# Kernel tuning notes

Measured on AMD Instinct MI355X. Metric: run time of the kernel, lower is better.

Reference implementation:

```python
import jax, jax.numpy as jnp
import numpy as np

L, N, D, E, KD = 4, 40000, 128, 320000, 16
DECAY, N_ITER, EPS = 0.5, 3, 1e-5


def setup_inputs() -> dict:
    key = jax.random.key(0)
    ks = jax.random.split(key, 16)
    s = 0.05
    return {
        "x": jax.random.normal(ks[0], (L, N, D), jnp.float32),
        "edge_rows": jax.random.randint(ks[1], (E,), 0, N, jnp.int32),
        "edge_cols": jax.random.randint(ks[2], (E,), 0, N, jnp.int32),
        "edge_vals": jax.random.uniform(ks[3], (E,), jnp.float32) * 0.1,
        "sage_W": jax.random.normal(ks[4], (D, D), jnp.float32) * s,
        "sage_b": jnp.zeros((D,), jnp.float32),
        "sage_agg_W": jax.random.normal(ks[5], (D, D), jnp.float32) * s,
        "key_W": jax.random.normal(ks[6], (D, KD), jnp.float32) * s,
        "query_W": jax.random.normal(ks[7], (D, KD), jnp.float32) * s,
        "value_W": jax.random.normal(ks[8], (D, D), jnp.float32) * s,
        "attn_ln_g": jnp.ones((D,), jnp.float32),
        "attn_ln_b": jnp.zeros((D,), jnp.float32),
        "lin_W": jax.random.normal(ks[9], (D, D), jnp.float32) * s,
        "lin_b": jnp.zeros((D,), jnp.float32),
        "ln_g": jnp.ones((D,), jnp.float32),
        "ln_b": jnp.zeros((D,), jnp.float32),
    }


def _layernorm(x, g, b):
    mu = jnp.mean(x, axis=-1, keepdims=True)
    var = jnp.mean((x - mu) ** 2, axis=-1, keepdims=True)
    return (x - mu) * jax.lax.rsqrt(var + EPS) * g + b


def _spmm(rows, cols, vals, x2d):
    # sparse [N,N] @ dense [N,F]: out[r] = sum_e vals[e] * x2d[cols[e]] for rows[e]==r
    return jax.ops.segment_sum(vals[:, None] * x2d[cols], rows, num_segments=N)


def reference(x, edge_rows, edge_cols, edge_vals, sage_W, sage_b, sage_agg_W,
              key_W, query_W, value_W, attn_ln_g, attn_ln_b,
              lin_W, lin_b, ln_g, ln_b):
    # x: [L, N, D]
    x2d = jnp.transpose(x, (1, 0, 2)).reshape(N, L * D)  # [N, L*D]

    # ---- SAGEConv ----
    proj = x @ sage_W + sage_b
    agg = _spmm(edge_rows, edge_cols, edge_vals, x2d)
    agg = jnp.transpose(agg.reshape(N, L, D), (1, 0, 2)) @ sage_agg_W
    sage_out = jax.nn.silu(proj + agg)

    # ---- RetentiveAttention ----
    weights = jnp.mean((x @ key_W) * (x @ query_W), axis=-1, keepdims=True)
    x_acc = x
    cur = x2d
    for _ in range(1, N_ITER):
        cur = _spmm(edge_rows, edge_cols, edge_vals, cur * DECAY)
        xr = jnp.transpose(cur.reshape(N, L, D), (1, 0, 2))  # [L, N, D]
        weights = weights + jnp.mean((xr @ key_W) * (xr @ query_W), axis=-1, keepdims=True)
        x_acc = x_acc + xr
    attn_out = _layernorm((x_acc @ value_W) * weights, attn_ln_g, attn_ln_b)

    # ---- GPSConv fusion ----
    y = jax.nn.silu((sage_out + attn_out) @ lin_W + lin_b)
    return _layernorm(y, ln_g, ln_b)
```

## Files before the change

### kernel.cpp

```cpp
#include <hip/hip_runtime.h>
#include <math.h>

#define LL 4
#define NN 40000
#define DD 128
#define EE 320000
#define ROWS (LL*NN)
#define ND (NN*DD)
#define EPS_LN 1e-5f

typedef __attribute__((ext_vector_type(8))) short bf16x8;
typedef __attribute__((ext_vector_type(4))) short s16x4;
typedef __attribute__((ext_vector_type(4))) float f32x4;

#define OFF_CNT      0
#define OFF_ROWPTR   40000
#define OFF_ROWOFS   80004
#define OFF_CCOLS    120004
#define OFF_CVALS    440004
#define OFF_WBF      760004
#define OFF_A        829636
#define OFF_B        (OFF_A + ROWS*DD/2)
#define OFF_XBF      (OFF_B + ROWS*DD/2)

#define WB_W0  0
#define WB_W1  32768
#define WB_WV  65536
#define WB_WL  98304
#define WB_K   131072
#define WB_Q   135168
#define WB_LO_BIG 16384
#define WB_LO_KQ  2048
#define WB_LOGICAL 69632

__device__ __forceinline__ unsigned fu(float f) { union { float f; unsigned u; } v; v.f = f; return v.u; }
__device__ __forceinline__ float uf(unsigned u) { union { unsigned u; float f; } v; v.u = u; return v.f; }

__device__ __forceinline__ short f2bf(float f) {
    unsigned u = fu(f);
    unsigned r = u + 0x7fffu + ((u >> 16) & 1u);
    return (short)(r >> 16);
}
__device__ __forceinline__ float bf2f(short h) { return uf(((unsigned)(unsigned short)h) << 16); }
__device__ __forceinline__ void splitbf(float v, short& h, short& l) {
    h = f2bf(v);
    l = f2bf(v - bf2f(h));
}

__device__ __forceinline__ unsigned pack_hi(float a, float b) {
    return (fu(a) >> 16) | (fu(b) & 0xffff0000u);
}
__device__ __forceinline__ float resid(float a) {
    return a - uf(fu(a) & 0xffff0000u);
}

union FragU { bf16x8 v; unsigned u[4]; };

__global__ void k_hist(const int* __restrict__ rows, int* __restrict__ cnt) {
    int e = blockIdx.x * 256 + threadIdx.x;
    if (e < EE) atomicAdd(&cnt[rows[e]], 1);
}

__global__ __launch_bounds__(1024) void k_scan1(const int* __restrict__ cnt,
                                                int* __restrict__ row_ptr,
                                                int* __restrict__ bsum) {
    __shared__ int wtot[16];
    int tid = threadIdx.x, lane = tid & 63, wid = tid >> 6;
    int i = blockIdx.x * 1024 + tid;
    int v = (i < NN) ? cnt[i] : 0;
    int incl = v;
    #pragma unroll
    for (int off = 1; off < 64; off <<= 1) {
        int t = __shfl_up(incl, off);
        if (lane >= off) incl += t;
    }
    if (lane == 63) wtot[wid] = incl;
    __syncthreads();
    if (wid == 0) {
        int wv = (lane < 16) ? wtot[lane] : 0;
        #pragma unroll
        for (int off = 1; off < 16; off <<= 1) {
            int t = __shfl_up(wv, off);
            if (lane >= off) wv += t;
        }
        if (lane < 16) wtot[lane] = wv;
    }
    __syncthreads();
    int excl = ((wid > 0) ? wtot[wid - 1] : 0) + incl - v;
    if (i < NN) row_ptr[i] = excl;
    if (tid == 0) bsum[blockIdx.x] = wtot[15];
}

__global__ void k_scan2(const int* __restrict__ bsum, int* __restrict__ bofs) {
    int lane = threadIdx.x;
    int v = (lane < 40) ? bsum[lane] : 0;
    int incl = v;
    #pragma unroll
    for (int off = 1; off < 64; off <<= 1) {
        int t = __shfl_up(incl, off);
        if (lane >= off) incl += t;
    }
    if (lane < 40) bofs[lane] = incl - v;
    if (lane == 39) bofs[40] = incl;
}

__global__ __launch_bounds__(1024) void k_scan3(const int* __restrict__ bofs,
                                                int* __restrict__ row_ptr,
                                                int* __restrict__ row_ofs) {
    int i = blockIdx.x * 1024 + threadIdx.x;
    int add = bofs[blockIdx.x];
    if (i < NN) {
        int v = row_ptr[i] + add;
        row_ptr[i] = v;
        row_ofs[i] = v;
    }
    if (i == NN) row_ptr[NN] = bofs[40];
}

__global__ void k_scatter(const int* __restrict__ rows, const int* __restrict__ cols,
                          const float* __restrict__ vals, int* __restrict__ row_ofs,
                          int* __restrict__ csr_cols, float* __restrict__ csr_vals) {
    int e = blockIdx.x * 256 + threadIdx.x;
    if (e < EE) {
        int r = rows[e];
        int p = atomicAdd(&row_ofs[r], 1);
        csr_cols[p] = cols[e];
        csr_vals[p] = vals[e];
    }
}

__global__ __launch_bounds__(256) void k_xcast(const float* __restrict__ x, short* __restrict__ o) {
    int t = blockIdx.x * 256 + threadIdx.x;
    int n = t >> 4;
    int d8 = (t & 15) * 8;
    #pragma unroll
    for (int l = 0; l < LL; ++l) {
        const float* xp = x + (size_t)l * ND + (size_t)n * 128 + d8;
        f32x4 a = *(const f32x4*)xp;
        f32x4 b = *(const f32x4*)(xp + 4);
        bf16x8 r;
        #pragma unroll
        for (int j = 0; j < 4; ++j) { r[j] = f2bf(a[j]); r[j + 4] = f2bf(b[j]); }
        *(bf16x8*)(o + (size_t)n * 512 + l * 128 + d8) = r;
    }
}

__global__ __launch_bounds__(256) void k_spmm(const short* __restrict__ in,
                                              const int* __restrict__ row_ptr,
                                              const int* __restrict__ ccols,
                                              const float* __restrict__ cvals,
                                              short* __restrict__ out) {
    int wid = blockIdx.x * 4 + (threadIdx.x >> 6);
    int rA = wid * 2;
    int lane = threadIdx.x & 63;
    const short* inl = in + lane * 8;
    float accA[8] = {0.f,0.f,0.f,0.f,0.f,0.f,0.f,0.f};
    float accB[8] = {0.f,0.f,0.f,0.f,0.f,0.f,0.f,0.f};
    int a0 = row_ptr[rA], a1 = row_ptr[rA + 1], b1 = row_ptr[rA + 2];
    int b0 = a1;
    while (a0 + 4 <= a1 && b0 + 4 <= b1) {
        int ca[4], cb[4]; float va[4], vb[4]; bf16x8 xa[4], xb[4];
        #pragma unroll
        for (int j = 0; j < 4; ++j) {
            ca[j] = ccols[a0 + j]; va[j] = cvals[a0 + j];
            cb[j] = ccols[b0 + j]; vb[j] = cvals[b0 + j];
        }
        #pragma unroll
        for (int j = 0; j < 4; ++j) {
            xa[j] = *(const bf16x8*)(inl + (size_t)ca[j] * 512);
            xb[j] = *(const bf16x8*)(inl + (size_t)cb[j] * 512);
        }
        #pragma unroll
        for (int j = 0; j < 4; ++j)
            #pragma unroll
            for (int k = 0; k < 8; ++k) {
                accA[k] += va[j] * bf2f(xa[j][k]);
                accB[k] += vb[j] * bf2f(xb[j][k]);
            }
        a0 += 4; b0 += 4;
    }
    #pragma unroll 1
    for (int pass = 0; pass < 2; ++pass) {
        int e = pass ? b0 : a0, e1 = pass ? b1 : a1;
        float* acc = pass ? accB : accA;
        for (; e + 4 <= e1; e += 4) {
            int cc[4]; float vv[4]; bf16x8 xv[4];
            #pragma unroll
            for (int j = 0; j < 4; ++j) { cc[j] = ccols[e + j]; vv[j] = cvals[e + j]; }
            #pragma unroll
            for (int j = 0; j < 4; ++j) xv[j] = *(const bf16x8*)(inl + (size_t)cc[j] * 512);
            #pragma unroll
            for (int j = 0; j < 4; ++j)
                #pragma unroll
                for (int k = 0; k < 8; ++k) acc[k] += vv[j] * bf2f(xv[j][k]);
        }
        for (; e < e1; ++e) {
            int c = ccols[e];
            float v = cvals[e];
            bf16x8 xv = *(const bf16x8*)(inl + (size_t)c * 512);
            #pragma unroll
            for (int k = 0; k < 8; ++k) acc[k] += v * bf2f(xv[k]);
        }
    }
    bf16x8 oA, oB;
    #pragma unroll
    for (int k = 0; k < 8; ++k) { oA[k] = f2bf(accA[k]); oB[k] = f2bf(accB[k]); }
    *(bf16x8*)(out + (size_t)rA * 512 + lane * 8) = oA;
    *(bf16x8*)(out + (size_t)(rA + 1) * 512 + lane * 8) = oB;
}

__global__ void k_prep(const float* __restrict__ W0, const float* __restrict__ W1,
                       const float* __restrict__ Wv, const float* __restrict__ Wl,
                       const float* __restrict__ Kw, const float* __restrict__ Qw,
                       short* __restrict__ o) {
    int t = blockIdx.x * 256 + threadIdx.x;
    if (t >= WB_LOGICAL) return;
    float v;
    int hi_idx, lo_idx;
    if (t < 65536) {
        int m = t >> 14, idx = t & 16383;
        int nn = idx >> 7, kk = idx & 127;
        const float* M = (m == 0) ? W0 : (m == 1) ? W1 : (m == 2) ? Wv : Wl;
        v = M[kk * 128 + nn];
        hi_idx = m * 32768 + idx;
        lo_idx = hi_idx + WB_LO_BIG;
    } else {
        int t2 = t - 65536;
        int sel = t2 >> 11;
        int idx = t2 & 2047;
        int nn = idx >> 7, kk = idx & 127;
        const float* M = sel ? Qw : Kw;
        v = M[kk * 16 + nn];
        hi_idx = WB_K + sel * 4096 + idx;
        lo_idx = hi_idx + WB_LO_KQ;
    }
    short h, l;
    splitbf(v, h, l);
    o[hi_idx] = h;
    o[lo_idx] = l;
}

#define MFMA(a, b, c) __builtin_amdgcn_mfma_f32_16x16x32_bf16(a, b, c, 0, 0, 0)

__global__ __launch_bounds__(256) void k_dense(
    const float* __restrict__ x, const short* __restrict__ A, const short* __restrict__ B,
    const short* __restrict__ wbf,
    const float* __restrict__ sage_b, const float* __restrict__ attn_g,
    const float* __restrict__ attn_b, const float* __restrict__ lin_b,
    const float* __restrict__ ln_g, const float* __restrict__ ln_b,
    float* __restrict__ out)
{
    __shared__ short pv[4][2][2048];
    const int tid = threadIdx.x;
    const int w = tid >> 6;
    const int lane = tid & 63;
    const int n = lane & 15;
    const int q = lane >> 4;
    const int rowA = blockIdx.x * 64 + w * 16 + n;
    const int l = rowA / NN;
    const int node = rowA - l * NN;
    char* pB = (char*)&pv[w][0][0];
    char* vB = (char*)&pv[w][1][0];

    bf16x8 xh[4], ah[4], ch[4];
    f32x4 kx = {0,0,0,0}, qx = {0,0,0,0};
    f32x4 ka = {0,0,0,0}, qa = {0,0,0,0};
    f32x4 kb = {0,0,0,0}, qb = {0,0,0,0};

    {
        const float* xp = x + (size_t)rowA * 128 + q * 8;
        const short* ap = A + (size_t)node * 512 + l * 128 + q * 8;
        const short* bp = B + (size_t)node * 512 + l * 128 + q * 8;
        const short* Kp = wbf + WB_K + n * 128 + q * 8;
        const short* Qp = wbf + WB_Q + n * 128 + q * 8;
        #pragma unroll
        for (int s = 0; s < 4; ++s) {
            f32x4 x0 = *(const f32x4*)(xp + s * 32);
            f32x4 x1 = *(const f32x4*)(xp + s * 32 + 4);
            bf16x8 av = *(const bf16x8*)(ap + s * 32);
            bf16x8 bv = *(const bf16x8*)(bp + s * 32);

            f32x4 c0, c1;
            #pragma unroll
            for (int j = 0; j < 4; ++j) {
                c0[j] = x0[j] + 0.5f * bf2f(av[j])     + 0.25f * bf2f(bv[j]);
                c1[j] = x1[j] + 0.5f * bf2f(av[j + 4]) + 0.25f * bf2f(bv[j + 4]);
            }

            FragU fxh, fxl, fch;
            #pragma unroll
            for (int i = 0; i < 2; ++i) {
                fxh.u[i]     = pack_hi(x0[2*i], x0[2*i+1]);
                fxh.u[i + 2] = pack_hi(x1[2*i], x1[2*i+1]);
                fxl.u[i]     = pack_hi(resid(x0[2*i]), resid(x0[2*i+1]));
                fxl.u[i + 2] = pack_hi(resid(x1[2*i]), resid(x1[2*i+1]));
                fch.u[i]     = pack_hi(c0[2*i], c0[2*i+1]);
                fch.u[i + 2] = pack_hi(c1[2*i], c1[2*i+1]);
            }
            xh[s] = fxh.v; ah[s] = av; ch[s] = fch.v;

            bf16x8 bkh = *(const bf16x8*)(Kp + s * 32);
            bf16x8 bkl = *(const bf16x8*)(Kp + WB_LO_KQ + s * 32);
            bf16x8 bqh = *(const bf16x8*)(Qp + s * 32);
            bf16x8 bql = *(const bf16x8*)(Qp + WB_LO_KQ + s * 32);
            kx = MFMA(fxh.v, bkh, kx); kx = MFMA(fxl.v, bkh, kx); kx = MFMA(fxh.v, bkl, kx);
            qx = MFMA(fxh.v, bqh, qx); qx = MFMA(fxl.v, bqh, qx); qx = MFMA(fxh.v, bql, qx);
            ka = MFMA(av, bkh, ka); qa = MFMA(av, bqh, qa);
            kb = MFMA(bv, bkh, kb); qb = MFMA(bv, bqh, qb);
        }
    }

    f32x4 wts;
    #pragma unroll
    for (int r = 0; r < 4; ++r) {
        float p = kx[r] * qx[r] + 0.25f * (ka[r] * qa[r]) + 0.0625f * (kb[r] * qb[r]);
        p += __shfl_xor(p, 1);
        p += __shfl_xor(p, 2);
        p += __shfl_xor(p, 4);
        p += __shfl_xor(p, 8);
        wts[r] = p * (1.f / 16.f);
    }

    #pragma unroll 1
    for (int h = 0; h < 2; ++h) {
        f32x4 S[4];
        #pragma unroll
        for (int t = 0; t < 4; ++t) {
            float bv = sage_b[(h * 4 + t) * 16 + n];
            S[t] = (f32x4){bv, bv, bv, bv};
        }
        #pragma unroll
        for (int s = 0; s < 4; ++s) {
            #pragma unroll
            for (int t = 0; t < 4; ++t) {
                int col = (h * 4 + t) * 16 + n;
                bf16x8 w0h = *(const bf16x8*)(wbf + WB_W0 + col * 128 + s * 32 + q * 8);
                S[t] = MFMA(xh[s], w0h, S[t]);
                bf16x8 w1h = *(const bf16x8*)(wbf + WB_W1 + col * 128 + s * 32 + q * 8);
                S[t] = MFMA(ah[s], w1h, S[t]);
            }
        }
        #pragma unroll
        for (int t = 0; t < 4; ++t)
            #pragma unroll
            for (int r = 0; r < 4; ++r) {
                float v = S[t][r];
                v = v / (1.f + __expf(-v));
                int row = q * 4 + r;
                int byte = (row * 256 + ((h * 4 + t) * 16 + n) * 2) ^ ((row & 7) << 4);
                *(short*)(pB + byte) = f2bf(v);
            }
    }
    asm volatile("" ::: "memory");

    float mu_n, rs_n;
    {
        f32x4 s1 = {0,0,0,0}, s2 = {0,0,0,0};
        #pragma unroll 1
        for (int h = 0; h < 2; ++h) {
            f32x4 V[4];
            #pragma unroll
            for (int t = 0; t < 4; ++t) V[t] = (f32x4){0.f, 0.f, 0.f, 0.f};
            #pragma unroll
            for (int s = 0; s < 4; ++s)
                #pragma unroll
                for (int t = 0; t < 4; ++t) {
                    int col = (h * 4 + t) * 16 + n;
                    bf16x8 wvh = *(const bf16x8*)(wbf + WB_WV + col * 128 + s * 32 + q * 8);
                    V[t] = MFMA(ch[s], wvh, V[t]);
                }
            #pragma unroll
            for (int t = 0; t < 4; ++t)
                #pragma unroll
                for (int r = 0; r < 4; ++r) {
                    float v = V[t][r] * wts[r];
                    s1[r] += v; s2[r] += v * v;
                    int row = q * 4 + r;
                    int byte = (row * 256 + ((h * 4 + t) * 16 + n) * 2) ^ ((row & 7) << 4);
                    *(short*)(vB + byte) = f2bf(v);
                }
        }
        #pragma unroll
        for (int r = 0; r < 4; ++r) {
            float a1 = s1[r], a2 = s2[r];
            a1 += __shfl_xor(a1, 1); a2 += __shfl_xor(a2, 1);
            a1 += __shfl_xor(a1, 2); a2 += __shfl_xor(a2, 2);
            a1 += __shfl_xor(a1, 4); a2 += __shfl_xor(a2, 4);
            a1 += __shfl_xor(a1, 8); a2 += __shfl_xor(a2, 8);
            s1[r] = a1; s2[r] = a2;
        }
        float mu4[4], rs4[4];
        #pragma unroll
        for (int r = 0; r < 4; ++r) {
            mu4[r] = s1[r] * (1.f / 128.f);
            float var = s2[r] * (1.f / 128.f) - mu4[r] * mu4[r];
            rs4[r] = rsqrtf(var + EPS_LN);
        }
        int src = (n >> 2) << 4;
        float mA = __shfl(mu4[0], src), mB_ = __shfl(mu4[1], src);
        float mC = __shfl(mu4[2], src), mD = __shfl(mu4[3], src);
        float rA = __shfl(rs4[0], src), rB_ = __shfl(rs4[1], src);
        float rC = __shfl(rs4[2], src), rD = __shfl(rs4[3], src);
        float m01 = (n & 1) ? mB_ : mA, m23 = (n & 1) ? mD : mC;
        float r01 = (n & 1) ? rB_ : rA, r23 = (n & 1) ? rD : rC;
        mu_n = (n & 2) ? m23 : m01;
        rs_n = (n & 2) ? r23 : r01;
    }
    asm volatile("" ::: "memory");

    bf16x8 zh[4];
    #pragma unroll
    for (int s = 0; s < 4; ++s) {
        int byte = (n * 256 + s * 64 + q * 16) ^ ((n & 7) << 4);
        bf16x8 ph = *(const bf16x8*)(pB + byte);
        bf16x8 vh = *(const bf16x8*)(vB + byte);
        const float* gp = attn_g + s * 32 + q * 8;
        const float* bp = attn_b + s * 32 + q * 8;
        f32x4 g0 = *(const f32x4*)gp, g1 = *(const f32x4*)(gp + 4);
        f32x4 b0 = *(const f32x4*)bp, b1 = *(const f32x4*)(bp + 4);
        float z[8];
        #pragma unroll
        for (int j = 0; j < 4; ++j) {
            z[j]     = bf2f(ph[j])     + (bf2f(vh[j])     - mu_n) * rs_n * g0[j] + b0[j];
            z[j + 4] = bf2f(ph[j + 4]) + (bf2f(vh[j + 4]) - mu_n) * rs_n * g1[j] + b1[j];
        }
        FragU f;
        f.u[0] = pack_hi(z[0], z[1]); f.u[1] = pack_hi(z[2], z[3]);
        f.u[2] = pack_hi(z[4], z[5]); f.u[3] = pack_hi(z[6], z[7]);
        zh[s] = f.v;
    }
    asm volatile("" ::: "memory");

    float* fz = (float*)pB;
    f32x4 t1 = {0,0,0,0}, t2 = {0,0,0,0};
    #pragma unroll 1
    for (int h = 0; h < 2; ++h) {
        f32x4 F[4];
        #pragma unroll
        for (int t = 0; t < 4; ++t) {
            float bv = lin_b[(h * 4 + t) * 16 + n];
            F[t] = (f32x4){bv, bv, bv, bv};
        }
        #pragma unroll
        for (int s = 0; s < 4; ++s)
            #pragma unroll
            for (int t = 0; t < 4; ++t) {
                int col = (h * 4 + t) * 16 + n;
                bf16x8 wlh = *(const bf16x8*)(wbf + WB_WL + col * 128 + s * 32 + q * 8);
                F[t] = MFMA(zh[s], wlh, F[t]);
            }
        #pragma unroll
        for (int t = 0; t < 4; ++t)
            #pragma unroll
            for (int r = 0; r < 4; ++r) {
                float v = F[t][r];
                v = v / (1.f + __expf(-v));
                t1[r] += v; t2[r] += v * v;
                fz[(q * 4 + r) * 128 + (h * 4 + t) * 16 + n] = v;
            }
    }
    asm volatile("" ::: "memory");
    #pragma unroll
    for (int r = 0; r < 4; ++r) {
        float a1 = t1[r], a2 = t2[r];
        a1 += __shfl_xor(a1, 1); a2 += __shfl_xor(a2, 1);
        a1 += __shfl_xor(a1, 2); a2 += __shfl_xor(a2, 2);
        a1 += __shfl_xor(a1, 4); a2 += __shfl_xor(a2, 4);
        a1 += __shfl_xor(a1, 8); a2 += __shfl_xor(a2, 8);
        t1[r] = a1; t2[r] = a2;
    }
    #pragma unroll
    for (int t = 0; t < 8; ++t) {
        float g = ln_g[t * 16 + n];
        float bb = ln_b[t * 16 + n];
        #pragma unroll
        for (int r = 0; r < 4; ++r) {
            float mu = t1[r] * (1.f / 128.f);
            float var = t2[r] * (1.f / 128.f) - mu * mu;
            float rs = rsqrtf(var + EPS_LN);
            float v = fz[(q * 4 + r) * 128 + t * 16 + n];
            size_t row = (size_t)blockIdx.x * 64 + w * 16 + q * 4 + r;
            out[row * 128 + t * 16 + n] = (v - mu) * rs * g + bb;
        }
    }
}

extern "C" void kernel_launch(void* const* d_in, const int* in_sizes, int n_in,
                              void* d_out, int out_size, void* d_ws, size_t ws_size,
                              hipStream_t stream) {
    const float* x       = (const float*)d_in[0];
    const int*   erows   = (const int*)d_in[1];
    const int*   ecols   = (const int*)d_in[2];
    const float* evals   = (const float*)d_in[3];
    const float* sage_W  = (const float*)d_in[4];
    const float* sage_b  = (const float*)d_in[5];
    const float* sage_aW = (const float*)d_in[6];
    const float* key_W   = (const float*)d_in[7];
    const float* query_W = (const float*)d_in[8];
    const float* value_W = (const float*)d_in[9];
    const float* attn_g  = (const float*)d_in[10];
    const float* attn_b  = (const float*)d_in[11];
    const float* lin_W   = (const float*)d_in[12];
    const float* lin_b   = (const float*)d_in[13];
    const float* ln_g    = (const float*)d_in[14];
    const float* ln_b    = (const float*)d_in[15];
    float* out = (float*)d_out;

    int*   wsi = (int*)d_ws;
    float* wsf = (float*)d_ws;
    int*   cnt      = wsi + OFF_CNT;
    int*   row_ptr  = wsi + OFF_ROWPTR;
    int*   row_ofs  = wsi + OFF_ROWOFS;
    int*   csr_cols = wsi + OFF_CCOLS;
    float* csr_vals = wsf + OFF_CVALS;
    short* wbf      = (short*)(wsf + OFF_WBF);
    short* Abf      = (short*)(wsf + OFF_A);
    short* Bbf      = (short*)(wsf + OFF_B);
    short* Xbf      = (short*)(wsf + OFF_XBF);
    int*   bsum     = (int*)(wsf + OFF_A);
    int*   bofs     = bsum + 64;

    hipMemsetAsync(cnt, 0, NN * sizeof(int), stream);
    k_hist<<<(EE + 255) / 256, 256, 0, stream>>>(erows, cnt);
    k_prep<<<(WB_LOGICAL + 255) / 256, 256, 0, stream>>>(sage_W, sage_aW, value_W, lin_W,
                                                         key_W, query_W, wbf);
    k_xcast<<<NN * 16 / 256, 256, 0, stream>>>(x, Xbf);
    k_scan1<<<40, 1024, 0, stream>>>(cnt, row_ptr, bsum);
    k_scan2<<<1, 64, 0, stream>>>(bsum, bofs);
    k_scan3<<<40, 1024, 0, stream>>>(bofs, row_ptr, row_ofs);
    k_scatter<<<(EE + 255) / 256, 256, 0, stream>>>(erows, ecols, evals, row_ofs, csr_cols, csr_vals);

    k_spmm<<<NN / 8, 256, 0, stream>>>(Xbf, row_ptr, csr_cols, csr_vals, Abf);
    k_spmm<<<NN / 8, 256, 0, stream>>>(Abf, row_ptr, csr_cols, csr_vals, Bbf);

    k_dense<<<ROWS / 64, 256, 0, stream>>>(x, Abf, Bbf, wbf, sage_b, attn_g, attn_b,
                                           lin_b, ln_g, ln_b, out);
}
```

Baseline: 550.0 us.

## Pre-swizzle weights into MFMA fragment order and keep dense intermediates in registers

Weight preparation now writes bf16 weights in per-lane fragment order, so each lane loads a contiguous 16-byte chunk at lane*8 with coalesced wave-wide loads instead of strided column reads. The dense kernel computes all 8 output tiles at once rather than two halves. The SAGE and value outputs and the final activation stay in registers, and the attention layernorm is applied before a single LDS transpose of z. This removes two LDS round trips and the global re-reads of the layernorm parameters, at the cost of more live registers and possibly lower occupancy.

```diff
diff --git a/kernel.cpp b/kernel.cpp
--- a/kernel.cpp
+++ b/kernel.cpp
@@ -219,10 +219,13 @@
     int hi_idx, lo_idx;
     if (t < 65536) {
         int m = t >> 14, idx = t & 16383;
-        int nn = idx >> 7, kk = idx & 127;
+        int col = idx >> 7, kk = idx & 127;
         const float* M = (m == 0) ? W0 : (m == 1) ? W1 : (m == 2) ? Wv : Wl;
-        v = M[kk * 128 + nn];
-        hi_idx = m * 32768 + idx;
+        v = M[kk * 128 + col];
+        int tt = col >> 4, nn = col & 15;
+        int s = kk >> 5, q = (kk >> 3) & 3, j = kk & 7;
+        int fm = (tt * 4 + s) * 512 + (q * 16 + nn) * 8 + j;
+        hi_idx = m * 32768 + fm;
         lo_idx = hi_idx + WB_LO_BIG;
     } else {
         int t2 = t - 65536;
@@ -231,7 +234,9 @@
         int nn = idx >> 7, kk = idx & 127;
         const float* M = sel ? Qw : Kw;
         v = M[kk * 16 + nn];
-        hi_idx = WB_K + sel * 4096 + idx;
+        int s = kk >> 5, q = (kk >> 3) & 3, j = kk & 7;
+        int fm = s * 512 + (q * 16 + nn) * 8 + j;
+        hi_idx = WB_K + sel * 4096 + fm;
         lo_idx = hi_idx + WB_LO_KQ;
     }
     short h, l;
@@ -250,7 +255,7 @@
     const float* __restrict__ ln_g, const float* __restrict__ ln_b,
     float* __restrict__ out)
 {
-    __shared__ short pv[4][2][2048];
+    __shared__ short zs[4][16 * 128];
     const int tid = threadIdx.x;
     const int w = tid >> 6;
     const int lane = tid & 63;
@@ -259,8 +264,8 @@
     const int rowA = blockIdx.x * 64 + w * 16 + n;
     const int l = rowA / NN;
     const int node = rowA - l * NN;
-    char* pB = (char*)&pv[w][0][0];
-    char* vB = (char*)&pv[w][1][0];
+    char* zb = (char*)&zs[0][0] + w * 4096;
+    const short* wl8 = wbf + lane * 8;
 
     bf16x8 xh[4], ah[4], ch[4];
     f32x4 kx = {0,0,0,0}, qx = {0,0,0,0};
@@ -271,8 +276,6 @@
         const float* xp = x + (size_t)rowA * 128 + q * 8;
         const short* ap = A + (size_t)node * 512 + l * 128 + q * 8;
         const short* bp = B + (size_t)node * 512 + l * 128 + q * 8;
-        const short* Kp = wbf + WB_K + n * 128 + q * 8;
-        const short* Qp = wbf + WB_Q + n * 128 + q * 8;
         #pragma unroll
         for (int s = 0; s < 4; ++s) {
             f32x4 x0 = *(const f32x4*)(xp + s * 32);
@@ -299,10 +302,10 @@
             }
             xh[s] = fxh.v; ah[s] = av; ch[s] = fch.v;
 
-            bf16x8 bkh = *(const bf16x8*)(Kp + s * 32);
-            bf16x8 bkl = *(const bf16x8*)(Kp + WB_LO_KQ + s * 32);
-            bf16x8 bqh = *(const bf16x8*)(Qp + s * 32);
-            bf16x8 bql = *(const bf16x8*)(Qp + WB_LO_KQ + s * 32);
+            bf16x8 bkh = *(const bf16x8*)(wl8 + WB_K + s * 512);
+            bf16x8 bkl = *(const bf16x8*)(wl8 + WB_K + WB_LO_KQ + s * 512);
+            bf16x8 bqh = *(const bf16x8*)(wl8 + WB_Q + s * 512);
+            bf16x8 bql = *(const bf16x8*)(wl8 + WB_Q + WB_LO_KQ + s * 512);
             kx = MFMA(fxh.v, bkh, kx); kx = MFMA(fxl.v, bkh, kx); kx = MFMA(fxh.v, bkl, kx);
             qx = MFMA(fxh.v, bqh, qx); qx = MFMA(fxl.v, bqh, qx); qx = MFMA(fxh.v, bql, qx);
             ka = MFMA(av, bkh, ka); qa = MFMA(av, bqh, qa);
@@ -321,145 +324,103 @@
         wts[r] = p * (1.f / 16.f);
     }
 
-    #pragma unroll 1
-    for (int h = 0; h < 2; ++h) {
-        f32x4 S[4];
-        #pragma unroll
-        for (int t = 0; t < 4; ++t) {
-            float bv = sage_b[(h * 4 + t) * 16 + n];
-            S[t] = (f32x4){bv, bv, bv, bv};
-        }
-        #pragma unroll
-        for (int s = 0; s < 4; ++s) {
-            #pragma unroll
-            for (int t = 0; t < 4; ++t) {
-                int col = (h * 4 + t) * 16 + n;
-                bf16x8 w0h = *(const bf16x8*)(wbf + WB_W0 + col * 128 + s * 32 + q * 8);
-                S[t] = MFMA(xh[s], w0h, S[t]);
-                bf16x8 w1h = *(const bf16x8*)(wbf + WB_W1 + col * 128 + s * 32 + q * 8);
-                S[t] = MFMA(ah[s], w1h, S[t]);
-            }
-        }
-        #pragma unroll
-        for (int t = 0; t < 4; ++t)
-            #pragma unroll
-            for (int r = 0; r < 4; ++r) {
-                float v = S[t][r];
-                v = v / (1.f + __expf(-v));
-                int row = q * 4 + r;
-                int byte = (row * 256 + ((h * 4 + t) * 16 + n) * 2) ^ ((row & 7) << 4);
-                *(short*)(pB + byte) = f2bf(v);
-            }
-    }
-    asm volatile("" ::: "memory");
-
-    float mu_n, rs_n;
-    {
-        f32x4 s1 = {0,0,0,0}, s2 = {0,0,0,0};
-        #pragma unroll 1
-        for (int h = 0; h < 2; ++h) {
-            f32x4 V[4];
-            #pragma unroll
-            for (int t = 0; t < 4; ++t) V[t] = (f32x4){0.f, 0.f, 0.f, 0.f};
-            #pragma unroll
-            for (int s = 0; s < 4; ++s)
-                #pragma unroll
-                for (int t = 0; t < 4; ++t) {
-                    int col = (h * 4 + t) * 16 + n;
-                    bf16x8 wvh = *(const bf16x8*)(wbf + WB_WV + col * 128 + s * 32 + q * 8);
-                    V[t] = MFMA(ch[s], wvh, V[t]);
-                }
-            #pragma unroll
-            for (int t = 0; t < 4; ++t)
-                #pragma unroll
-                for (int r = 0; r < 4; ++r) {
-                    float v = V[t][r] * wts[r];
-                    s1[r] += v; s2[r] += v * v;
-                    int row = q * 4 + r;
-                    int byte = (row * 256 + ((h * 4 + t) * 16 + n) * 2) ^ ((row & 7) << 4);
-                    *(short*)(vB + byte) = f2bf(v);
-                }
-        }
+    f32x4 S[8];
+    #pragma unroll
+    for (int t = 0; t < 8; ++t) {
+        float bv = sage_b[t * 16 + n];
+        S[t] = (f32x4){bv, bv, bv, bv};
+    }
+    #pragma unroll
+    for (int s = 0; s < 4; ++s) {
+        #pragma unroll
+        for (int t = 0; t < 8; ++t) {
+            bf16x8 w0h = *(const bf16x8*)(wl8 + WB_W0 + (t * 4 + s) * 512);
+            S[t] = MFMA(xh[s], w0h, S[t]);
+            bf16x8 w1h = *(const bf16x8*)(wl8 + WB_W1 + (t * 4 + s) * 512);
+            S[t] = MFMA(ah[s], w1h, S[t]);
+        }
+    }
+    #pragma unroll
+    for (int t = 0; t < 8; ++t)
         #pragma unroll
         for (int r = 0; r < 4; ++r) {
-            float a1 = s1[r], a2 = s2[r];
-            a1 += __shfl_xor(a1, 1); a2 += __shfl_xor(a2, 1);
-            a1 += __shfl_xor(a1, 2); a2 += __shfl_xor(a2, 2);
-            a1 += __shfl_xor(a1, 4); a2 += __shfl_xor(a2, 4);
-            a1 += __shfl_xor(a1, 8); a2 += __shfl_xor(a2, 8);
-            s1[r] = a1; s2[r] = a2;
-        }
-        float mu4[4], rs4[4];
+            float v = S[t][r];
+            S[t][r] = v / (1.f + __expf(-v));
+        }
+
+    f32x4 V[8];
+    #pragma unroll
+    for (int t = 0; t < 8; ++t) V[t] = (f32x4){0.f, 0.f, 0.f, 0.f};
+    #pragma unroll
+    for (int s = 0; s < 4; ++s)
+        #pragma unroll
+        for (int t = 0; t < 8; ++t) {
+            bf16x8 wvh = *(const bf16x8*)(wl8 + WB_WV + (t * 4 + s) * 512);
+            V[t] = MFMA(ch[s], wvh, V[t]);
+        }
+    f32x4 s1 = {0,0,0,0}, s2 = {0,0,0,0};
+    #pragma unroll
+    for (int t = 0; t < 8; ++t)
         #pragma unroll
         for (int r = 0; r < 4; ++r) {
-            mu4[r] = s1[r] * (1.f / 128.f);
-            float var = s2[r] * (1.f / 128.f) - mu4[r] * mu4[r];
-            rs4[r] = rsqrtf(var + EPS_LN);
-        }
-        int src = (n >> 2) << 4;
-        float mA = __shfl(mu4[0], src), mB_ = __shfl(mu4[1], src);
-        float mC = __shfl(mu4[2], src), mD = __shfl(mu4[3], src);
-        float rA = __shfl(rs4[0], src), rB_ = __shfl(rs4[1], src);
-        float rC = __shfl(rs4[2], src), rD = __shfl(rs4[3], src);
-        float m01 = (n & 1) ? mB_ : mA, m23 = (n & 1) ? mD : mC;
-        float r01 = (n & 1) ? rB_ : rA, r23 = (n & 1) ? rD : rC;
-        mu_n = (n & 2) ? m23 : m01;
-        rs_n = (n & 2) ? r23 : r01;
-    }
-    asm volatile("" ::: "memory");
+            float v = V[t][r] * wts[r];
+            V[t][r] = v;
+            s1[r] += v; s2[r] += v * v;
+        }
+    #pragma unroll
+    for (int r = 0; r < 4; ++r) {
+        float a1 = s1[r], a2 = s2[r];
+        a1 += __shfl_xor(a1, 1); a2 += __shfl_xor(a2, 1);
+        a1 += __shfl_xor(a1, 2); a2 += __shfl_xor(a2, 2);
+        a1 += __shfl_xor(a1, 4); a2 += __shfl_xor(a2, 4);
+        a1 += __shfl_xor(a1, 8); a2 += __shfl_xor(a2, 8);
+        s1[r] = a1; s2[r] = a2;
+    }
+    #pragma unroll
+    for (int t = 0; t < 8; ++t) {
+        float g = attn_g[t * 16 + n];
+        float bb = attn_b[t * 16 + n];
+        #pragma unroll
+        for (int r = 0; r < 4; ++r) {
+            float mu = s1[r] * (1.f / 128.f);
+            float var = s2[r] * (1.f / 128.f) - mu * mu;
+            float rs = rsqrtf(var + EPS_LN);
+            float zval = S[t][r] + (V[t][r] - mu) * rs * g + bb;
+            int row = q * 4 + r;
+            int byte = (row * 256 + (t * 16 + n) * 2) ^ ((row & 7) << 4);
+            *(short*)(zb + byte) = f2bf(zval);
+        }
+    }
 
     bf16x8 zh[4];
     #pragma unroll
     for (int s = 0; s < 4; ++s) {
         int byte = (n * 256 + s * 64 + q * 16) ^ ((n & 7) << 4);
-        bf16x8 ph = *(const bf16x8*)(pB + byte);
-        bf16x8 vh = *(const bf16x8*)(vB + byte);
-        const float* gp = attn_g + s * 32 + q * 8;
-        const float* bp = attn_b + s * 32 + q * 8;
-        f32x4 g0 = *(const f32x4*)gp, g1 = *(const f32x4*)(gp + 4);
-        f32x4 b0 = *(const f32x4*)bp, b1 = *(const f32x4*)(bp + 4);
-        float z[8];
-        #pragma unroll
-        for (int j = 0; j < 4; ++j) {
-            z[j]     = bf2f(ph[j])     + (bf2f(vh[j])     - mu_n) * rs_n * g0[j] + b0[j];
-            z[j + 4] = bf2f(ph[j + 4]) + (bf2f(vh[j + 4]) - mu_n) * rs_n * g1[j] + b1[j];
-        }
-        FragU f;
-        f.u[0] = pack_hi(z[0], z[1]); f.u[1] = pack_hi(z[2], z[3]);
-        f.u[2] = pack_hi(z[4], z[5]); f.u[3] = pack_hi(z[6], z[7]);
-        zh[s] = f.v;
-    }
-    asm volatile("" ::: "memory");
-
-    float* fz = (float*)pB;
+        zh[s] = *(const bf16x8*)(zb + byte);
+    }
+    f32x4 F[8];
+    #pragma unroll
+    for (int t = 0; t < 8; ++t) {
+        float bv = lin_b[t * 16 + n];
+        F[t] = (f32x4){bv, bv, bv, bv};
+    }
+    #pragma unroll
+    for (int s = 0; s < 4; ++s)
+        #pragma unroll
+        for (int t = 0; t < 8; ++t) {
+            bf16x8 wlh = *(const bf16x8*)(wl8 + WB_WL + (t * 4 + s) * 512);
+            F[t] = MFMA(zh[s], wlh, F[t]);
+        }
     f32x4 t1 = {0,0,0,0}, t2 = {0,0,0,0};
-    #pragma unroll 1
-    for (int h = 0; h < 2; ++h) {
-        f32x4 F[4];
-        #pragma unroll
-        for (int t = 0; t < 4; ++t) {
-            float bv = lin_b[(h * 4 + t) * 16 + n];
-            F[t] = (f32x4){bv, bv, bv, bv};
-        }
-        #pragma unroll
-        for (int s = 0; s < 4; ++s)
-            #pragma unroll
-            for (int t = 0; t < 4; ++t) {
-                int col = (h * 4 + t) * 16 + n;
-                bf16x8 wlh = *(const bf16x8*)(wbf + WB_WL + col * 128 + s * 32 + q * 8);
-                F[t] = MFMA(zh[s], wlh, F[t]);
-            }
-        #pragma unroll
-        for (int t = 0; t < 4; ++t)
-            #pragma unroll
-            for (int r = 0; r < 4; ++r) {
-                float v = F[t][r];
-                v = v / (1.f + __expf(-v));
-                t1[r] += v; t2[r] += v * v;
-                fz[(q * 4 + r) * 128 + (h * 4 + t) * 16 + n] = v;
-            }
-    }
-    asm volatile("" ::: "memory");
+    #pragma unroll
+    for (int t = 0; t < 8; ++t)
+        #pragma unroll
+        for (int r = 0; r < 4; ++r) {
+            float v = F[t][r];
+            v = v / (1.f + __expf(-v));
+            F[t][r] = v;
+            t1[r] += v; t2[r] += v * v;
+        }
     #pragma unroll
     for (int r = 0; r < 4; ++r) {
         float a1 = t1[r], a2 = t2[r];
@@ -478,9 +439,8 @@
             float mu = t1[r] * (1.f / 128.f);
             float var = t2[r] * (1.f / 128.f) - mu * mu;
             float rs = rsqrtf(var + EPS_LN);
-            float v = fz[(q * 4 + r) * 128 + t * 16 + n];
             size_t row = (size_t)blockIdx.x * 64 + w * 16 + q * 4 + r;
-            out[row * 128 + t * 16 + n] = (v - mu) * rs * g + bb;
+            out[row * 128 + t * 16 + n] = (F[t][r] - mu) * rs * g + bb;
         }
     }
 }
```

New measurement: 503.3 us. 8.5% less time.
